# Kernel optimization log

Hardware: AMD Instinct MI355X
Metric: run time of the kernel (lower is better)

## Reference

```python
import jax, jax.numpy as jnp
import numpy as np

B, D, NH, HD = 32, 384, 8, 48
HP = WP = 14
N = HP * WP
L = 24
EPS_LN = 1e-5


def _ln(x, w, b):
    m = jnp.mean(x, -1, keepdims=True)
    v = jnp.mean((x - m) ** 2, -1, keepdims=True)
    return (x - m) * jax.lax.rsqrt(v + EPS_LN) * w + b


def _gelu(x):
    return jax.nn.gelu(x, approximate=False)


def _conv(x, w, s, p, groups=1):
    return jax.lax.conv_general_dilated(x, w, (s, s), [(p, p), (p, p)],
        dimension_numbers=('NCHW', 'OIHW', 'NCHW'), feature_group_count=groups)


def _bn(x, g, b):
    # eval-mode BatchNorm2d with running_mean=0, running_var=1
    scale = g * jax.lax.rsqrt(jnp.asarray(1.0 + 1e-5, x.dtype))
    return x * scale[None, :, None, None] + b[None, :, None, None]


def _pos_embed(pos_w, pos_b):
    two_pi = 2.0 * np.pi
    y = (jnp.arange(HP, dtype=jnp.float32) + 1.0) / ((HP + 1e-6) * two_pi)
    xg = (jnp.arange(WP, dtype=jnp.float32) + 1.0) / ((WP + 1e-6) * two_pi)
    y_embed = jnp.broadcast_to(y[:, None], (HP, WP))
    x_embed = jnp.broadcast_to(xg[None, :], (HP, WP))
    dim_t = 10000.0 ** (2.0 * (jnp.arange(32) // 2).astype(jnp.float32) / 32.0)
    px = x_embed[..., None] / dim_t  # [H,W,32]
    py = y_embed[..., None] / dim_t
    px = jnp.stack([jnp.sin(px[..., 0::2]), jnp.cos(px[..., 1::2])], -1).reshape(HP, WP, 32)
    py = jnp.stack([jnp.sin(py[..., 0::2]), jnp.cos(py[..., 1::2])], -1).reshape(HP, WP, 32)
    pos = jnp.concatenate([py, px], -1)  # [H,W,64]
    pos = jnp.einsum('hwc,dc->hwd', pos, pos_w[:, :, 0, 0]) + pos_b
    return pos.reshape(1, N, D)


def _xca_block(t, p):
    Bc = t.shape[0]
    h = _ln(t, p['n1_w'], p['n1_b'])
    qkv = (h @ p['qkv_w'].T + p['qkv_b']).reshape(Bc, N, 3, NH, HD)
    q = qkv[:, :, 0].transpose(0, 2, 3, 1)  # [B,H,d,N]
    k = qkv[:, :, 1].transpose(0, 2, 3, 1)
    v = qkv[:, :, 2].transpose(0, 2, 3, 1)
    q = q / jnp.maximum(jnp.linalg.norm(q, axis=-1, keepdims=True), 1e-12)
    k = k / jnp.maximum(jnp.linalg.norm(k, axis=-1, keepdims=True), 1e-12)
    attn = jnp.einsum('bhdn,bhen->bhde', q, k) * p['temp'][None, :, None, None]
    a = jax.nn.softmax(attn, -1)  # channel-wise softmax over d_h
    o = jnp.einsum('bhde,bhen->bnhd', a, v).reshape(Bc, N, D)
    o = o @ p['proj_w'].T + p['proj_b']
    t = t + p['g1'] * o
    h = _ln(t, p['n3_w'], p['n3_b']).transpose(0, 2, 1).reshape(Bc, D, HP, WP)
    h = _conv(h, p['lpi1_w'], 1, 1, groups=D) + p['lpi1_b'][None, :, None, None]
    h = _bn(_gelu(h), p['lpi_bn_g'], p['lpi_bn_b'])
    h = _conv(h, p['lpi2_w'], 1, 1, groups=D) + p['lpi2_b'][None, :, None, None]
    t = t + p['g3'] * h.reshape(Bc, D, N).transpose(0, 2, 1)
    h = _ln(t, p['n2_w'], p['n2_b'])
    h = _gelu(h @ p['fc1_w'].T + p['fc1_b']) @ p['fc2_w'].T + p['fc2_b']
    return t + p['g2'] * h


def _ca_block(t, p):
    Bc, Nc, _ = t.shape
    h = _ln(t, p['n1_w'], p['n1_b'])
    qkv = (h @ p['qkv_w'].T + p['qkv_b']).reshape(Bc, Nc, 3, NH, HD)
    q = qkv[:, :, 0].transpose(0, 2, 1, 3)  # [B,H,N,d]
    k = qkv[:, :, 1].transpose(0, 2, 1, 3)
    v = qkv[:, :, 2].transpose(0, 2, 1, 3)
    attn = jnp.sum(q[:, :, :1] * k, -1) * (HD ** -0.5)  # [B,H,N]
    a = jax.nn.softmax(attn, -1)
    cls = jnp.einsum('bhn,bhnd->bhd', a, v).reshape(Bc, 1, D)
    cls = cls @ p['proj_w'].T + p['proj_b']
    attn_out = jnp.concatenate([cls, h[:, 1:]], 1)
    t = t + p['g1'] * attn_out
    t = _ln(t, p['n2_w'], p['n2_b'])
    res = t
    cls2 = _gelu(t[:, :1] @ p['fc1_w'].T + p['fc1_b']) @ p['fc2_w'].T + p['fc2_b']
    return jnp.concatenate([p['g2'] * cls2, t[:, 1:]], 1) + res


def setup_inputs() -> dict:
    key = jax.random.key(0)
    k = iter(jax.random.split(key, 64))
    def rn(shape, std=0.02):
        return jax.random.normal(next(k), shape, jnp.float32) * std
    inp = {}
    inp['x'] = jax.random.normal(next(k), (B, 3, 224, 224), jnp.float32)
    inp['cls_token'] = rn((1, 1, D))
    inp['pos_w'] = rn((D, 64, 1, 1))
    inp['pos_b'] = jnp.zeros((D,))
    for i, (co, ci) in enumerate([(48, 3), (96, 48), (192, 96), (384, 192)], 1):
        inp['pe_w%d' % i] = rn((co, ci, 3, 3))
        inp['pe_g%d' % i] = jnp.ones((co,))
        inp['pe_b%d' % i] = jnp.zeros((co,))
    inp['xqkv_w'] = rn((L, 3 * D, D)); inp['xqkv_b'] = jnp.zeros((L, 3 * D))
    inp['xproj_w'] = rn((L, D, D)); inp['xproj_b'] = jnp.zeros((L, D))
    inp['xtemp'] = jnp.ones((L, NH))
    for n in ('n1', 'n2', 'n3'):
        inp['x%s_w' % n] = jnp.ones((L, D)); inp['x%s_b' % n] = jnp.zeros((L, D))
    inp['xfc1_w'] = rn((L, 4 * D, D)); inp['xfc1_b'] = jnp.zeros((L, 4 * D))
    inp['xfc2_w'] = rn((L, D, 4 * D)); inp['xfc2_b'] = jnp.zeros((L, D))
    inp['xlpi1_w'] = rn((L, D, 1, 3, 3), 0.1); inp['xlpi1_b'] = jnp.zeros((L, D))
    inp['xlpi2_w'] = rn((L, D, 1, 3, 3), 0.1); inp['xlpi2_b'] = jnp.zeros((L, D))
    inp['xbn_g'] = jnp.ones((L, D)); inp['xbn_b'] = jnp.zeros((L, D))
    for g in ('g1', 'g2', 'g3'):
        inp['x%s' % g] = jnp.full((L, D), 1e-5)
    L2 = 2
    inp['cqkv_w'] = rn((L2, 3 * D, D)); inp['cqkv_b'] = jnp.zeros((L2, 3 * D))
    inp['cproj_w'] = rn((L2, D, D)); inp['cproj_b'] = jnp.zeros((L2, D))
    for n in ('n1', 'n2'):
        inp['c%s_w' % n] = jnp.ones((L2, D)); inp['c%s_b' % n] = jnp.zeros((L2, D))
    inp['cfc1_w'] = rn((L2, 4 * D, D)); inp['cfc1_b'] = jnp.zeros((L2, 4 * D))
    inp['cfc2_w'] = rn((L2, D, 4 * D)); inp['cfc2_b'] = jnp.zeros((L2, D))
    inp['cg1'] = jnp.full((L2, D), 1e-5); inp['cg2'] = jnp.full((L2, D), 1e-5)
    inp['norm_w'] = jnp.ones((D,)); inp['norm_b'] = jnp.zeros((D,))
    inp['head_w'] = rn((1000, D)); inp['head_b'] = jnp.zeros((1000,))
    return inp


def reference(x, cls_token, pos_w, pos_b, pe_w1, pe_g1, pe_b1, pe_w2, pe_g2, pe_b2, pe_w3, pe_g3, pe_b3, pe_w4, pe_g4, pe_b4, xqkv_w, xqkv_b, xproj_w, xproj_b, xtemp, xn1_w, xn1_b, xn2_w, xn2_b, xn3_w, xn3_b, xfc1_w, xfc1_b, xfc2_w, xfc2_b, xlpi1_w, xlpi1_b, xlpi2_w, xlpi2_b, xbn_g, xbn_b, xg1, xg2, xg3, cqkv_w, cqkv_b, cproj_w, cproj_b, cn1_w, cn1_b, cn2_w, cn2_b, cfc1_w, cfc1_b, cfc2_w, cfc2_b, cg1, cg2, norm_w, norm_b, head_w, head_b):
    h = _gelu(_bn(_conv(x, pe_w1, 2, 1), pe_g1, pe_b1))
    h = _gelu(_bn(_conv(h, pe_w2, 2, 1), pe_g2, pe_b2))
    h = _gelu(_bn(_conv(h, pe_w3, 2, 1), pe_g3, pe_b3))
    h = _bn(_conv(h, pe_w4, 2, 1), pe_g4, pe_b4)  # [B,D,14,14]
    t = h.reshape(h.shape[0], D, N).transpose(0, 2, 1)  # [B,N,D]
    t = t + _pos_embed(pos_w, pos_b)
    xca = {'qkv_w': xqkv_w, 'qkv_b': xqkv_b, 'proj_w': xproj_w, 'proj_b': xproj_b,
           'temp': xtemp, 'n1_w': xn1_w, 'n1_b': xn1_b, 'n2_w': xn2_w, 'n2_b': xn2_b,
           'n3_w': xn3_w, 'n3_b': xn3_b, 'fc1_w': xfc1_w, 'fc1_b': xfc1_b,
           'fc2_w': xfc2_w, 'fc2_b': xfc2_b, 'lpi1_w': xlpi1_w, 'lpi1_b': xlpi1_b,
           'lpi2_w': xlpi2_w, 'lpi2_b': xlpi2_b, 'lpi_bn_g': xbn_g, 'lpi_bn_b': xbn_b,
           'g1': xg1, 'g2': xg2, 'g3': xg3}
    t, _ = jax.lax.scan(lambda c, p: (_xca_block(c, p), None), t, xca)
    t = jnp.concatenate([jnp.broadcast_to(cls_token, (t.shape[0], 1, D)), t], 1)
    for i in range(2):
        p = {'qkv_w': cqkv_w[i], 'qkv_b': cqkv_b[i], 'proj_w': cproj_w[i],
             'proj_b': cproj_b[i], 'n1_w': cn1_w[i], 'n1_b': cn1_b[i],
             'n2_w': cn2_w[i], 'n2_b': cn2_b[i], 'fc1_w': cfc1_w[i],
             'fc1_b': cfc1_b[i], 'fc2_w': cfc2_w[i], 'fc2_b': cfc2_b[i],
             'g1': cg1[i], 'g2': cg2[i]}
        t = _ca_block(t, p)
    t = _ln(t, norm_w, norm_b)[:, 0]
    return t @ head_w.T + head_b
```

## Files before the change

### kernel.cpp

```cpp
#include <hip/hip_runtime.h>
#include <hip/hip_bf16.h>

#define B_ 32
#define D_ 384
#define N_ 196
#define NH_ 8
#define HD_ 48
#define L_ 24

typedef __bf16 bf16x8 __attribute__((ext_vector_type(8)));
typedef __bf16 bf16x4 __attribute__((ext_vector_type(4)));
typedef float f32x4 __attribute__((ext_vector_type(4)));

__device__ __forceinline__ float gelu_f(float v){
    return 0.5f * v * (1.0f + erff(v * 0.70710678118654752f));
}

__global__ __launch_bounds__(256) void cvt_bf(const float* __restrict__ s, __bf16* __restrict__ d, long n){
    long i = ((long)blockIdx.x * 256 + threadIdx.x) * 8;
    if (i >= n) return;
    float4 a = *reinterpret_cast<const float4*>(s + i);
    float4 b = *reinterpret_cast<const float4*>(s + i + 4);
    bf16x8 r;
    r[0] = (__bf16)a.x; r[1] = (__bf16)a.y; r[2] = (__bf16)a.z; r[3] = (__bf16)a.w;
    r[4] = (__bf16)b.x; r[5] = (__bf16)b.y; r[6] = (__bf16)b.z; r[7] = (__bf16)b.w;
    *reinterpret_cast<bf16x8*>(d + i) = r;
}

__global__ __launch_bounds__(256) void cvt_pad(const float* __restrict__ s, __bf16* __restrict__ d,
                                               int rows, int K, int rows_pad){
    int id = blockIdx.x * 256 + threadIdx.x;
    if (id >= rows_pad * K) return;
    int r = id / K;
    d[id] = (r < rows) ? (__bf16)s[id] : (__bf16)0.f;
}

__global__ __launch_bounds__(256) void wprep(const float* __restrict__ w, __bf16* __restrict__ W2,
                                             int Co, int Ci, int Kpad){
    int id = blockIdx.x * 256 + threadIdx.x;
    if (id >= Co * Kpad) return;
    int co = id / Kpad, k = id - co * Kpad;
    float v = 0.f;
    if (k < 9 * Ci){
        int tap = k / Ci, ci = k - tap * Ci;
        v = w[((long)co * Ci + ci) * 9 + tap];
    }
    W2[id] = (__bf16)v;
}

__global__ __launch_bounds__(256) void im2col_x(const float* __restrict__ x, __bf16* __restrict__ A){
    int id = blockIdx.x * 256 + threadIdx.x;
    if (id >= 401408) return;
    int ox = id % 112; int t1 = id / 112; int oy = t1 % 112; int b = t1 / 112;
    __bf16 buf[32];
    #pragma unroll
    for (int i = 0; i < 32; i++) buf[i] = (__bf16)0.f;
    const float* xb = x + (long)b * 3 * 224 * 224;
    #pragma unroll
    for (int tap = 0; tap < 9; tap++){
        int ky = tap / 3, kx = tap % 3;
        int iy = oy * 2 - 1 + ky, ix = ox * 2 - 1 + kx;
        if ((unsigned)iy < 224u && (unsigned)ix < 224u){
            #pragma unroll
            for (int ci = 0; ci < 3; ci++)
                buf[tap * 3 + ci] = (__bf16)xb[((long)ci * 224 + iy) * 224 + ix];
        }
    }
    __bf16* dst = A + (long)id * 32;
    #pragma unroll
    for (int i = 0; i < 4; i++)
        *reinterpret_cast<bf16x8*>(dst + i * 8) = *reinterpret_cast<bf16x8*>(buf + i * 8);
}

__global__ __launch_bounds__(256) void im2col_bf(const __bf16* __restrict__ in, __bf16* __restrict__ A,
                                                 int C, int Hi, int Wi, int Ho, int Wo, int Kpad, int total){
    int id = blockIdx.x * 256 + threadIdx.x;
    if (id >= total) return;
    int tap = id % 9; int pix = id / 9;
    int ox = pix % Wo; int t1 = pix / Wo; int oy = t1 % Ho; int b = t1 / Ho;
    int ky = tap / 3, kx = tap % 3;
    int iy = oy * 2 - 1 + ky, ix = ox * 2 - 1 + kx;
    __bf16* dst = A + (long)pix * Kpad + tap * C;
    if ((unsigned)iy < (unsigned)Hi && (unsigned)ix < (unsigned)Wi){
        const __bf16* src = in + ((long)(b * Hi + iy) * Wi + ix) * C;
        for (int c = 0; c < C; c += 8)
            *reinterpret_cast<bf16x8*>(dst + c) = *reinterpret_cast<const bf16x8*>(src + c);
    } else {
        bf16x8 z{};
        for (int c = 0; c < C; c += 8) *reinterpret_cast<bf16x8*>(dst + c) = z;
    }
    if (tap == 0){
        bf16x8 z{};
        for (int c = 9 * C; c < Kpad; c += 8)
            *reinterpret_cast<bf16x8*>(A + (long)pix * Kpad + c) = z;
    }
}

template<int GELU, int POSOUT>
__global__ __launch_bounds__(256) void gemm_conv(const __bf16* __restrict__ A, int Kpad,
                                                 const __bf16* __restrict__ W,
                                                 const float* __restrict__ g, const float* __restrict__ bb,
                                                 void* __restrict__ Cv, int N,
                                                 const float* __restrict__ pos){
    __shared__ __align__(16) char smem[20480];
    char* Ab = smem;
    char* Bb = smem + 10240;
    const int tid  = threadIdx.x;
    const int lane = tid & 63;
    const int wn   = (tid >> 6) & 1;
    const int wm   = tid >> 7;
    const int row0 = blockIdx.x * 128;
    const int col0 = blockIdx.y * 128;
    const int hi = lane >> 4, lo = lane & 15;
    f32x4 acc[4][4] = {};
    auto loadA = [&](int kk, int i)->bf16x8 {
        int p = i * 256 + tid;
        int r = p >> 2, cq = p & 3;
// ... 142 lines not shown
            int c = c0 + j;
            yb[(long)c * 196] = (__bf16)((v[j] - m) * r * n3w[c] + n3b[c]);
        }
    }
}

__global__ __launch_bounds__(128) void ln2res(float* __restrict__ t,
                                              const __bf16* __restrict__ hadd,
                                              const float* __restrict__ n2w, const float* __restrict__ n2b,
                                              __bf16* __restrict__ h){
    long row = blockIdx.x;
    int tid = threadIdx.x;
    int c0 = tid * 4;
    float v[4] = {0.f, 0.f, 0.f, 0.f};
    if (tid < 96){
        float4 tv = *reinterpret_cast<const float4*>(t + row * 384 + c0);
        bf16x4 hv = *reinterpret_cast<const bf16x4*>(hadd + row * 384 + c0);
        v[0] = tv.x + (float)hv[0];
        v[1] = tv.y + (float)hv[1];
        v[2] = tv.z + (float)hv[2];
        v[3] = tv.w + (float)hv[3];
        *reinterpret_cast<float4*>(t + row * 384 + c0) = make_float4(v[0], v[1], v[2], v[3]);
    }
    float s = v[0] + v[1] + v[2] + v[3];
    float ss = v[0] * v[0] + v[1] * v[1] + v[2] * v[2] + v[3] * v[3];
    for (int off = 32; off; off >>= 1){ s += __shfl_down(s, off); ss += __shfl_down(ss, off); }
    __shared__ float rs[2], rss[2];
    if ((tid & 63) == 0){ rs[tid >> 6] = s; rss[tid >> 6] = ss; }
    __syncthreads();
    float S = rs[0] + rs[1], SS = rss[0] + rss[1];
    float m = S * (1.0f / 384.0f);
    float var = SS * (1.0f / 384.0f) - m * m;
    float r = rsqrtf(var + 1e-5f);
    if (tid < 96){
        bf16x4 o;
        #pragma unroll
        for (int j = 0; j < 4; j++){
            int c = c0 + j;
            o[j] = (__bf16)((v[j] - m) * r * n2w[c] + n2b[c]);
        }
        *reinterpret_cast<bf16x4*>(h + row * 384 + c0) = o;
    }
}

__global__ __launch_bounds__(128) void fc2_res_ln(const __bf16* __restrict__ f2,
                                                  const float* __restrict__ g2,
                                                  float* __restrict__ t,
                                                  const float* __restrict__ n1w, const float* __restrict__ n1b,
                                                  __bf16* __restrict__ h){
    long row = blockIdx.x;
    int tid = threadIdx.x;
    int c0 = tid * 4;
    float v[4] = {0.f, 0.f, 0.f, 0.f};
    if (tid < 96){
        float4 tv = *reinterpret_cast<const float4*>(t + row * 384 + c0);
        bf16x4 fv = *reinterpret_cast<const bf16x4*>(f2 + row * 384 + c0);
        v[0] = tv.x + g2[c0 + 0] * (float)fv[0];
        v[1] = tv.y + g2[c0 + 1] * (float)fv[1];
        v[2] = tv.z + g2[c0 + 2] * (float)fv[2];
        v[3] = tv.w + g2[c0 + 3] * (float)fv[3];
        *reinterpret_cast<float4*>(t + row * 384 + c0) = make_float4(v[0], v[1], v[2], v[3]);
    }
    float s = v[0] + v[1] + v[2] + v[3];
    float ss = v[0] * v[0] + v[1] * v[1] + v[2] * v[2] + v[3] * v[3];
    for (int off = 32; off; off >>= 1){ s += __shfl_down(s, off); ss += __shfl_down(ss, off); }
    __shared__ float rs[2], rss[2];
    if ((tid & 63) == 0){ rs[tid >> 6] = s; rss[tid >> 6] = ss; }
    __syncthreads();
    float S = rs[0] + rs[1], SS = rss[0] + rss[1];
    float m = S * (1.0f / 384.0f);
    float var = SS * (1.0f / 384.0f) - m * m;
    float r = rsqrtf(var + 1e-5f);
    if (tid < 96){
        bf16x4 o;
        #pragma unroll
        for (int j = 0; j < 4; j++){
            int c = c0 + j;
            o[j] = (__bf16)((v[j] - m) * r * n1w[c] + n1b[c]);
        }
        *reinterpret_cast<bf16x4*>(h + row * 384 + c0) = o;
    }
}

template<int MODE, int OUTBF, int ACVT, int GUARD, int NGUARD>
__global__ __launch_bounds__(256) void gemm_bb2(const void* __restrict__ Av, long lda,
                                                const __bf16* __restrict__ W, int Kw,
                                                const float* __restrict__ bias,
                                                void* __restrict__ Cv, long ldc,
                                                int K, int M, int Ncols){
    __shared__ __align__(16) char smem[27648];
    char* Ab = smem;
    char* Bb = smem + 9216;
    const int tid = threadIdx.x;
    const int lane = tid & 63;
    const int wn = tid >> 6;
    const int row0 = blockIdx.x * 64;
    const int col0 = blockIdx.y * 128;
    const int hi = lane >> 4, lo = lane & 15;
    const __bf16* Abf = (const __bf16*)Av;
    const float* Af = (const float*)Av;
    f32x4 acc[4][2] = {};
    auto loadA = [&](int kk, int i)->bf16x8 {
        int p = i * 256 + tid;
        int r = p >> 3, cq = p & 7;
        bf16x8 va{};
        int grow = row0 + r;
        if (!GUARD || grow < M){
            long ai = (long)grow * lda + kk + cq * 8;
            if (ACVT){
                float4 a0 = *reinterpret_cast<const float4*>(Af + ai);
                float4 a1 = *reinterpret_cast<const float4*>(Af + ai + 4);
                va[0] = (__bf16)a0.x; va[1] = (__bf16)a0.y; va[2] = (__bf16)a0.z; va[3] = (__bf16)a0.w;
                va[4] = (__bf16)a1.x; va[5] = (__bf16)a1.y; va[6] = (__bf16)a1.z; va[7] = (__bf16)a1.w;
            } else {
                va = *reinterpret_cast<const bf16x8*>(Abf + ai);
            }
        }
        return va;
    };
    auto loadB = [&](int kk, int i)->bf16x8 {
        int p = i * 256 + tid;
        int r = p >> 3, cq = p & 7;
        return *reinterpret_cast<const bf16x8*>(W + (long)(col0 + r) * Kw + kk + cq * 8);
    };
    bf16x8 vaC[2], vwC[4];
    vaC[0] = loadA(0, 0); vaC[1] = loadA(0, 1);
    #pragma unroll
    for (int i = 0; i < 4; i++) vwC[i] = loadB(0, i);
    for (int k0 = 0; k0 < K; k0 += 64){
        #pragma unroll
        for (int i = 0; i < 2; i++){
            int p = i * 256 + tid;
            int r = p >> 3, cq = p & 7;
            *reinterpret_cast<bf16x8*>(Ab + r * 144 + cq * 16) = vaC[i];
        }
        #pragma unroll
        for (int i = 0; i < 4; i++){
            int p = i * 256 + tid;
            int r = p >> 3, cq = p & 7;
            *reinterpret_cast<bf16x8*>(Bb + r * 144 + cq * 16) = vwC[i];
        }
        __syncthreads();
        int kn = (k0 + 64 < K) ? k0 + 64 : k0;
        bf16x8 vaN[2], vwN[4];
        vaN[0] = loadA(kn, 0); vaN[1] = loadA(kn, 1);
        #pragma unroll
        for (int i = 0; i < 4; i++) vwN[i] = loadB(kn, i);
        bf16x8 af[2][4], bfr[2][2];
        #pragma unroll
        for (int m = 0; m < 4; m++){
            af[0][m] = *reinterpret_cast<const bf16x8*>(Ab + (m * 16 + lo) * 144 + hi * 16);
            af[1][m] = *reinterpret_cast<const bf16x8*>(Ab + (m * 16 + lo) * 144 + 64 + hi * 16);
        }
        #pragma unroll
        for (int n = 0; n < 2; n++){
            bfr[0][n] = *reinterpret_cast<const bf16x8*>(Bb + (wn * 32 + n * 16 + lo) * 144 + hi * 16);
            bfr[1][n] = *reinterpret_cast<const bf16x8*>(Bb + (wn * 32 + n * 16 + lo) * 144 + 64 + hi * 16);
        }
        #pragma unroll
        for (int kc = 0; kc < 2; kc++)
            #pragma unroll
            for (int m = 0; m < 4; m++)
                #pragma unroll
                for (int n = 0; n < 2; n++)
                    acc[m][n] = __builtin_amdgcn_mfma_f32_16x16x32_bf16(af[kc][m], bfr[kc][n], acc[m][n], 0, 0, 0);
        __syncthreads();
        vaC[0] = vaN[0]; vaC[1] = vaN[1];
        #pragma unroll
        for (int i = 0; i < 4; i++) vwC[i] = vwN[i];
    }
    float* Cf = (float*)Cv;
    __bf16* Cb = (__bf16*)Cv;
    #pragma unroll
    for (int m = 0; m < 4; m++){
        #pragma unroll
        for (int n = 0; n < 2; n++){
            int row = row0 + m * 16 + hi * 4;
            int col = col0 + wn * 32 + n * 16 + lo;
            if (NGUARD && col >= Ncols) continue;
            float bv = bias[col];
            #pragma unroll
            for (int j = 0; j < 4; j++){
                if (GUARD && (row + j) >= M) continue;
                float v = acc[m][n][j] + bv;
                if (MODE == 1) v = gelu_f(v);
                long ci = (long)(row + j) * ldc + col;
                if (OUTBF) Cb[ci] = (__bf16)v;
                else Cf[ci] = v;
            }
        }
    }
}

__global__ __launch_bounds__(256) void gemm_bb3(const __bf16* __restrict__ A, long lda,
                                                const __bf16* __restrict__ W, int Kw,
                                                const float* __restrict__ bias,
                                                __bf16* __restrict__ C, long ldc,
                                                int K){
    __shared__ __align__(16) char smem[18432];
    char* Ab = smem;
    char* Bb = smem + 9216;
    const int tid = threadIdx.x;
    const int lane = tid & 63;
    const int wid = tid >> 6;
    const int wm = wid >> 1, wnn = wid & 1;
    const int row0 = blockIdx.x * 64;
    const int col0 = blockIdx.y * 64;
    const int hi = lane >> 4, lo = lane & 15;
    f32x4 acc[2][2] = {};
    auto loadA = [&](int kk, int i)->bf16x8 {
        int p = i * 256 + tid;
        int r = p >> 3, cq = p & 7;
        return *reinterpret_cast<const bf16x8*>(A + (long)(row0 + r) * lda + kk + cq * 8);
    };
    auto loadB = [&](int kk, int i)->bf16x8 {
        int p = i * 256 + tid;
        int r = p >> 3, cq = p & 7;
        return *reinterpret_cast<const bf16x8*>(W + (long)(col0 + r) * Kw + kk + cq * 8);
    };
    bf16x8 vaC[2], vwC[2];
    vaC[0] = loadA(0, 0); vaC[1] = loadA(0, 1);
    vwC[0] = loadB(0, 0); vwC[1] = loadB(0, 1);
    for (int k0 = 0; k0 < K; k0 += 64){
        #pragma unroll
        for (int i = 0; i < 2; i++){
            int p = i * 256 + tid;
            int r = p >> 3, cq = p & 7;
            *reinterpret_cast<bf16x8*>(Ab + r * 144 + cq * 16) = vaC[i];
            *reinterpret_cast<bf16x8*>(Bb + r * 144 + cq * 16) = vwC[i];
        }
        __syncthreads();
        int kn = (k0 + 64 < K) ? k0 + 64 : k0;
        bf16x8 vaN[2], vwN[2];
        vaN[0] = loadA(kn, 0); vaN[1] = loadA(kn, 1);
        vwN[0] = loadB(kn, 0); vwN[1] = loadB(kn, 1);
        bf16x8 af[2][2], bfr[2][2];
        #pragma unroll
        for (int m = 0; m < 2; m++){
            af[0][m] = *reinterpret_cast<const bf16x8*>(Ab + (wm * 32 + m * 16 + lo) * 144 + hi * 16);
            af[1][m] = *reinterpret_cast<const bf16x8*>(Ab + (wm * 32 + m * 16 + lo) * 144 + 64 + hi * 16);
        }
        #pragma unroll
        for (int n = 0; n < 2; n++){
            bfr[0][n] = *reinterpret_cast<const bf16x8*>(Bb + (wnn * 32 + n * 16 + lo) * 144 + hi * 16);
            bfr[1][n] = *reinterpret_cast<const bf16x8*>(Bb + (wnn * 32 + n * 16 + lo) * 144 + 64 + hi * 16);
        }
        #pragma unroll
        for (int kc = 0; kc < 2; kc++)
            #pragma unroll
            for (int m = 0; m < 2; m++)
                #pragma unroll
                for (int n = 0; n < 2; n++)
                    acc[m][n] = __builtin_amdgcn_mfma_f32_16x16x32_bf16(af[kc][m], bfr[kc][n], acc[m][n], 0, 0, 0);
        __syncthreads();
        vaC[0] = vaN[0]; vaC[1] = vaN[1]; vwC[0] = vwN[0]; vwC[1] = vwN[1];
    }
    #pragma unroll
    for (int m = 0; m < 2; m++){
        #pragma unroll
        for (int n = 0; n < 2; n++){
            int row = row0 + wm * 32 + m * 16 + hi * 4;
            int col = col0 + wnn * 32 + n * 16 + lo;
            float bv = bias[col];
            #pragma unroll
            for (int j = 0; j < 4; j++)
                C[(long)(row + j) * ldc + col] = (__bf16)(acc[m][n][j] + bv);
        }
    }
}

__global__ __launch_bounds__(384) void pos_embed(const float* __restrict__ pw, const float* __restrict__ pb,
                                                 float* __restrict__ pos){
    __shared__ float p64[64];
    int n = blockIdx.x;
    int iy = n / 14, ix = n % 14;
    int t = threadIdx.x;
    if (t < 64){
        int axis = t >> 5;
        int c = t & 31;
        int u = c >> 1;
        float coord = (axis == 0) ? (float)(iy + 1) : (float)(ix + 1);
        float val = coord / ((14.0f + 1e-6f) * 6.283185307179586f);
        float T = powf(10000.0f, (float)u / 16.0f);
        float a = val / T;
        p64[t] = (c & 1) ? cosf(a) : sinf(a);
    }
    __syncthreads();
    float acc = 0.f;
    const float* wr = pw + (long)t * 64;
    #pragma unroll 8
    for (int c = 0; c < 64; c++) acc += p64[c] * wr[c];
    pos[n * 384 + t] = acc + pb[t];
}

__global__ __launch_bounds__(256) void xca2(const __bf16* __restrict__ qkv, const float* __restrict__ temp,
                                            __bf16* __restrict__ o){
    __shared__ __align__(16) char smem[45056];
    __bf16* qs = (__bf16*)smem;
    __bf16* ks = (__bf16*)(smem + 22272);
    float* inq = (float*)(smem + 44544);
    float* ink = (float*)(smem + 44736);
    float* att = (float*)smem;
    __bf16* abf = (__bf16*)(smem + 22272);
    int bh = blockIdx.x;
    int b = bh >> 3, h = bh & 7;
    const int tid = threadIdx.x;
    const int wid = tid >> 6, lane = tid & 63;
    const int hi = lane >> 4, lo = lane & 15;
    const __bf16* base = qkv + ((long)b * 196) * 1152 + h * 48;
    bf16x8 z8 = {};
    for (int idx = tid; idx < 48 * 28; idx += 256){
        int d = idx / 28, n = 196 + idx % 28;
        qs[d * 232 + n] = (__bf16)0.f;
        ks[d * 232 + n] = (__bf16)0.f;
    }
    for (int ch = tid; ch < 196 * 6; ch += 256){
        int n = ch / 6, c = ch % 6, d0 = c * 8;
        bf16x8 q8 = *reinterpret_cast<const bf16x8*>(base + (long)n * 1152 + d0);
        bf16x8 k8 = *reinterpret_cast<const bf16x8*>(base + (long)n * 1152 + 384 + d0);
        #pragma unroll
        for (int j = 0; j < 8; j++){
            qs[(d0 + j) * 232 + n] = q8[j];
            ks[(d0 + j) * 232 + n] = k8[j];
        }
    }
    __syncthreads();
    for (int r = wid; r < 48; r += 4){
        float sq = 0.f, sk = 0.f;
        for (int n = lane; n < 196; n += 64){
            float qv = (float)qs[r * 232 + n];
            float kv = (float)ks[r * 232 + n];
            sq += qv * qv; sk += kv * kv;
        }
        for (int off = 32; off; off >>= 1){ sq += __shfl_down(sq, off); sk += __shfl_down(sk, off); }
        if (lane == 0){
            inq[r] = 1.0f / fmaxf(sqrtf(sq), 1e-12f);
            ink[r] = 1.0f / fmaxf(sqrtf(sk), 1e-12f);
        }
    }
    __syncthreads();
    float tempv = temp[h];
    f32x4 qk0 = {}, qk1 = {}, qk2 = {};
    __builtin_amdgcn_s_setprio(1);
    {
        int mi = wid / 3, ni = wid % 3;
        #pragma unroll
        for (int k0 = 0; k0 < 224; k0 += 32){
            bf16x8 af = *reinterpret_cast<const bf16x8*>(qs + (mi * 16 + lo) * 232 + k0 + hi * 8);
            bf16x8 bf = *reinterpret_cast<const bf16x8*>(ks + (ni * 16 + lo) * 232 + k0 + hi * 8);
            qk0 = __builtin_amdgcn_mfma_f32_16x16x32_bf16(af, bf, qk0, 0, 0, 0);
        }
    }
    {
        int tt = wid + 4;
        int mi = tt / 3, ni = tt % 3;
        #pragma unroll
        for (int k0 = 0; k0 < 224; k0 += 32){
            bf16x8 af = *reinterpret_cast<const bf16x8*>(qs + (mi * 16 + lo) * 232 + k0 + hi * 8);
            bf16x8 bf = *reinterpret_cast<const bf16x8*>(ks + (ni * 16 + lo) * 232 + k0 + hi * 8);
            qk1 = __builtin_amdgcn_mfma_f32_16x16x32_bf16(af, bf, qk1, 0, 0, 0);
        }
    }
    if (wid == 0){
        #pragma unroll
        for (int k0 = 0; k0 < 224; k0 += 32){
            bf16x8 af = *reinterpret_cast<const bf16x8*>(qs + (2 * 16 + lo) * 232 + k0 + hi * 8);
            bf16x8 bf = *reinterpret_cast<const bf16x8*>(ks + (2 * 16 + lo) * 232 + k0 + hi * 8);
            qk2 = __builtin_amdgcn_mfma_f32_16x16x32_bf16(af, bf, qk2, 0, 0, 0);
        }
    }
    __builtin_amdgcn_s_setprio(0);
    __syncthreads();
    {
        int mi = wid / 3, ni = wid % 3;
        int e = ni * 16 + lo;
        float se = ink[e] * tempv;
        #pragma unroll
        for (int j = 0; j < 4; j++){
            int d = mi * 16 + hi * 4 + j;
            att[d * 68 + e] = qk0[j] * inq[d] * se;
        }
    }
    {
        int tt = wid + 4;
        int mi = tt / 3, ni = tt % 3;
        int e = ni * 16 + lo;
        float se = ink[e] * tempv;
        #pragma unroll
        for (int j = 0; j < 4; j++){
            int d = mi * 16 + hi * 4 + j;
            att[d * 68 + e] = qk1[j] * inq[d] * se;
        }
    }
    if (wid == 0){
        int e = 2 * 16 + lo;
        float se = ink[e] * tempv;
        #pragma unroll
        for (int j = 0; j < 4; j++){
            int d = 2 * 16 + hi * 4 + j;
            att[d * 68 + e] = qk2[j] * inq[d] * se;
        }
    }
    __syncthreads();
    if (tid < 192){
        int r = tid >> 2, q4 = tid & 3;
        const float* row = att + r * 68 + q4 * 12;
        float mx = -1e30f;
        #pragma unroll
        for (int i = 0; i < 12; i++) mx = fmaxf(mx, row[i]);
        mx = fmaxf(mx, __shfl_xor(mx, 1));
        mx = fmaxf(mx, __shfl_xor(mx, 2));
        float pv[12]; float sm = 0.f;
        #pragma unroll
        for (int i = 0; i < 12; i++){ pv[i] = expf(row[i] - mx); sm += pv[i]; }
        sm += __shfl_xor(sm, 1);
        sm += __shfl_xor(sm, 2);
        float inv = 1.0f / sm;
        #pragma unroll
        for (int i = 0; i < 12; i++) abf[r * 72 + q4 * 12 + i] = (__bf16)(pv[i] * inv);
    }
    for (int idx = tid; idx < 48 * 3; idx += 256){
        int r = idx / 3, c = 48 + (idx % 3) * 8;
        *reinterpret_cast<bf16x8*>(abf + r * 72 + c) = z8;
    }
    __syncthreads();
    __bf16* ob = o + ((long)b * 196) * 384 + h * 48;
    __builtin_amdgcn_s_setprio(1);
    for (int tt = wid; tt < 39; tt += 4){
        int mi = tt / 13, ni = tt % 13;
        int nB = ni * 16 + lo;
        const __bf16* vrow = base + (long)nB * 1152 + 768;
        f32x4 acc = {};
        #pragma unroll
        for (int e0 = 0; e0 < 64; e0 += 32){
            bf16x8 af = *reinterpret_cast<const bf16x8*>(abf + (mi * 16 + lo) * 72 + e0 + hi * 8);
            bf16x8 bf = *reinterpret_cast<const bf16x8*>(vrow + e0 + hi * 8);
            acc = __builtin_amdgcn_mfma_f32_16x16x32_bf16(af, bf, acc, 0, 0, 0);
        }
        int n = nB;
        if (n < 196){
            #pragma unroll
            for (int j = 0; j < 4; j++){
                int d = mi * 16 + hi * 4 + j;
                ob[(long)n * 384 + d] = (__bf16)acc[j];
            }
        }
    }
    __builtin_amdgcn_s_setprio(0);
}

__global__ __launch_bounds__(256) void lpi_g(const __bf16* __restrict__ ht,
                                             const float* __restrict__ w1, const float* __restrict__ b1,
                                             const float* __restrict__ bng, const float* __restrict__ bnb,
                                             const float* __restrict__ w2, const float* __restrict__ b2,
                                             const float* __restrict__ g3, __bf16* __restrict__ hadd){
    int bd = blockIdx.x;
    int d = bd % 384, b = bd / 384;
    __shared__ float p[16][16];
    __shared__ float p2[16][16];
    __shared__ float wA[9], wB[9];
    int tt = threadIdx.x;
    int yy = tt / 16, xx = tt % 16;
    p[yy][xx] = 0.f; p2[yy][xx] = 0.f;
    if (tt < 9){ wA[tt] = w1[d * 9 + tt]; wB[tt] = w2[d * 9 + tt]; }
    __syncthreads();
    if (tt < 196){
        int y = tt / 14, x = tt % 14;
        p[y + 1][x + 1] = (float)ht[((long)b * 384 + d) * 196 + tt];
    }
    __syncthreads();
    if (tt < 196){
        int y = tt / 14, x = tt % 14;
        float a = 0.f;
        #pragma unroll
        for (int ky = 0; ky < 3; ky++)
            #pragma unroll
            for (int kx = 0; kx < 3; kx++)
                a += wA[ky * 3 + kx] * p[y + ky][x + kx];
        a += b1[d];
        a = gelu_f(a);
        a = a * (bng[d] * rsqrtf(1.0f + 1e-5f)) + bnb[d];
        p2[y + 1][x + 1] = a;
    }
    __syncthreads();
    if (tt < 196){
        int y = tt / 14, x = tt % 14;
        float a = 0.f;
        #pragma unroll
        for (int ky = 0; ky < 3; ky++)
            #pragma unroll
            for (int kx = 0; kx < 3; kx++)
                a += wB[ky * 3 + kx] * p2[y + ky][x + kx];
        a += b2[d];
        hadd[((long)b * 196 + tt) * 384 + d] = (__bf16)(g3[d] * a);
    }
}

__global__ __launch_bounds__(256) void concat_cls(const float* __restrict__ t, const float* __restrict__ clstok,
                                                  float* __restrict__ tc){
    long i = (long)blockIdx.x * 256 + threadIdx.x;
    if (i >= (long)B_ * 197 * 384) return;
    int d = (int)(i % 384);
    long bn = i / 384;
    int n = (int)(bn % 197);
    int b = (int)(bn / 197);
    tc[i] = (n == 0) ? clstok[d] : t[((long)b * 196 + (n - 1)) * 384 + d];
}

__global__ __launch_bounds__(256) void ca_attn(const __bf16* __restrict__ qkv, float* __restrict__ clsp){
    int bh = blockIdx.x;
    int b = bh >> 3, h = bh & 7;
    const __bf16* base = qkv + (long)b * 197 * 1152 + h * 48;
    __shared__ float q0[48];
    __shared__ float at2[197];
    __shared__ float smax, ssum;
    int tid = threadIdx.x;
    if (tid < 48) q0[tid] = (float)base[tid];
    __syncthreads();
    if (tid < 197){
        const __bf16* kr = base + (long)tid * 1152 + 384;
        float s = 0.f;
        for (int d = 0; d < 48; d++) s += q0[d] * (float)kr[d];
        at2[tid] = s * rsqrtf(48.0f);
    }
    __syncthreads();
    if (tid == 0){
        float m = -1e30f;
// ... 36 lines not shown
    int d = (int)(i % 384);
    long bn = i / 384;
    int n = (int)(bn % 197);
    int b = (int)(bn / 197);
    float hv = hc[i];
    tc[i] = (n == 0) ? (g2[d] * cls2[b * 384 + d] + hv) : (hv + hv);
}

extern "C" void kernel_launch(void* const* d_in, const int* in_sizes, int n_in,
                              void* d_out, int out_size, void* d_ws, size_t ws_size,
                              hipStream_t stream){
    (void)in_sizes; (void)n_in; (void)out_size; (void)ws_size;
    const float* x      = (const float*)d_in[0];
    const float* clstok = (const float*)d_in[1];
    const float* pos_w  = (const float*)d_in[2];
    const float* pos_b  = (const float*)d_in[3];
    const float* pe_w[4] = {(const float*)d_in[4], (const float*)d_in[7], (const float*)d_in[10], (const float*)d_in[13]};
    const float* pe_g[4] = {(const float*)d_in[5], (const float*)d_in[8], (const float*)d_in[11], (const float*)d_in[14]};
    const float* pe_b[4] = {(const float*)d_in[6], (const float*)d_in[9], (const float*)d_in[12], (const float*)d_in[15]};
    const float* xqkv_w = (const float*)d_in[16];
    const float* xqkv_b = (const float*)d_in[17];
    const float* xproj_w = (const float*)d_in[18];
    const float* xproj_b = (const float*)d_in[19];
    const float* xtemp  = (const float*)d_in[20];
    const float* xn1_w = (const float*)d_in[21];
    const float* xn1_b = (const float*)d_in[22];
    const float* xn2_w = (const float*)d_in[23];
    const float* xn2_b = (const float*)d_in[24];
    const float* xn3_w = (const float*)d_in[25];
    const float* xn3_b = (const float*)d_in[26];
    const float* xfc1_w = (const float*)d_in[27];
    const float* xfc1_b = (const float*)d_in[28];
    const float* xfc2_w = (const float*)d_in[29];
    const float* xfc2_b = (const float*)d_in[30];
    const float* xlpi1_w = (const float*)d_in[31];
    const float* xlpi1_b = (const float*)d_in[32];
    const float* xlpi2_w = (const float*)d_in[33];
    const float* xlpi2_b = (const float*)d_in[34];
    const float* xbn_g = (const float*)d_in[35];
    const float* xbn_b = (const float*)d_in[36];
    const float* xg1 = (const float*)d_in[37];
    const float* xg2 = (const float*)d_in[38];
    const float* xg3 = (const float*)d_in[39];
    const float* cqkv_w = (const float*)d_in[40];
    const float* cqkv_b = (const float*)d_in[41];
    const float* cproj_w = (const float*)d_in[42];
    const float* cproj_b = (const float*)d_in[43];
    const float* cn1_w = (const float*)d_in[44];
    const float* cn1_b = (const float*)d_in[45];
    const float* cn2_w = (const float*)d_in[46];
    const float* cn2_b = (const float*)d_in[47];
    const float* cfc1_w = (const float*)d_in[48];
    const float* cfc1_b = (const float*)d_in[49];
    const float* cfc2_w = (const float*)d_in[50];
    const float* cfc2_b = (const float*)d_in[51];
    const float* cg1 = (const float*)d_in[52];
    const float* cg2 = (const float*)d_in[53];
    const float* norm_w = (const float*)d_in[54];
    const float* norm_b = (const float*)d_in[55];
    const float* head_w = (const float*)d_in[56];
    const float* head_b = (const float*)d_in[57];
    float* outp = (float*)d_out;

    float* ws = (float*)d_ws;
    __bf16* A1   = (__bf16*)(ws);
    __bf16* A2   = (__bf16*)(ws);
    __bf16* A3   = (__bf16*)(ws);
    __bf16* A4   = (__bf16*)(ws);
    __bf16* out1 = (__bf16*)(ws + 22500000L);
    __bf16* out2 = (__bf16*)(ws + 22500000L);
    __bf16* out3 = (__bf16*)(ws + 27400000L);
    __bf16* wcv  = (__bf16*)(ws + 36000000L);
    __bf16* W1c = wcv;
    __bf16* W2c = wcv + 1536;
    __bf16* W3c = wcv + 44544;
    __bf16* W4c = wcv + 216576;
    __bf16* wqkv_bf = (__bf16*)(ws);
    __bf16* wproj_bf = (__bf16*)(ws + 5308416L);
    __bf16* wfc1_bf = (__bf16*)(ws + 7077888L);
    __bf16* wfc2_bf = (__bf16*)(ws + 14155776L);
    float*  t       = ws + 21233664L;
    float*  pos     = ws + 23642112L;
    __bf16* h_bf    = (__bf16*)(ws + 23717376L);
    __bf16* qkv_bf  = (__bf16*)(ws + 24921600L);
    __bf16* o_bf    = (__bf16*)(ws + 28534272L);
    __bf16* ht_bf   = (__bf16*)(ws + 29738496L);
    __bf16* f1_bf   = (__bf16*)(ws + 32146944L);
    __bf16* o2_bf   = (__bf16*)(ws + 34555392L);
    __bf16* f2_bf   = (__bf16*)(ws + 24921600L);
    __bf16* hadd_bf = (__bf16*)(ws + 28534272L);
    float* tc   = ws;
    float* hc   = ws + 2420736L;
    __bf16* qkvc_bf = (__bf16*)(ws + 4841472L);
    float* clsp = ws + 8472576L;
    float* clso = clsp + 12288;
    float* f1c  = clso + 12288;
    float* cls2 = f1c + 49152;
    float* clsf = cls2 + 12288;
    __bf16* cqkv_bf  = (__bf16*)(ws + 9000000L);
    __bf16* cproj_bf = (__bf16*)(ws + 9500000L);
    __bf16* cfc1_bf  = (__bf16*)(ws + 9800000L);
    __bf16* cfc2_bf  = (__bf16*)(ws + 10400000L);
    __bf16* headw_bf = (__bf16*)(ws + 11000000L);

    wprep<<<(48 * 32 + 255) / 256, 256, 0, stream>>>(pe_w[0], W1c, 48, 3, 32);
    wprep<<<(96 * 448 + 255) / 256, 256, 0, stream>>>(pe_w[1], W2c, 96, 48, 448);
    wprep<<<(192 * 896 + 255) / 256, 256, 0, stream>>>(pe_w[2], W3c, 192, 96, 896);
    wprep<<<(384 * 1728 + 255) / 256, 256, 0, stream>>>(pe_w[3], W4c, 384, 192, 1728);

    im2col_x<<<1568, 256, 0, stream>>>(x, A1);
    { dim3 g(3136, 1); gemm_conv<1, 0><<<g, 256, 0, stream>>>(A1, 32, W1c, pe_g[0], pe_b[0], out1, 48, nullptr); }
    im2col_bf<<<(100352 * 9 + 255) / 256, 256, 0, stream>>>(out1, A2, 48, 112, 112, 56, 56, 448, 100352 * 9);
    { dim3 g(784, 1); gemm_conv<1, 0><<<g, 256, 0, stream>>>(A2, 448, W2c, pe_g[1], pe_b[1], out2, 96, nullptr); }
    im2col_bf<<<(25088 * 9 + 255) / 256, 256, 0, stream>>>(out2, A3, 96, 56, 56, 28, 28, 896, 25088 * 9);
    pos_embed<<<196, 384, 0, stream>>>(pos_w, pos_b, pos);
    { dim3 g(196, 2); gemm_conv<1, 0><<<g, 256, 0, stream>>>(A3, 896, W3c, pe_g[2], pe_b[2], out3, 192, nullptr); }
    im2col_bf<<<(6272 * 9 + 255) / 256, 256, 0, stream>>>(out3, A4, 192, 28, 28, 14, 14, 1728, 6272 * 9);
    { dim3 g(49, 3); gemm_conv<0, 1><<<g, 256, 0, stream>>>(A4, 1728, W4c, pe_g[3], pe_b[3], t, 384, pos); }

    {
        long n1 = (long)L_ * 1152 * 384;
        long n2 = (long)L_ * 384 * 384;
        long n3 = (long)L_ * 1536 * 384;
        cvt_bf<<<(int)((n1 + 2047) / 2048), 256, 0, stream>>>(xqkv_w, wqkv_bf, n1);
        cvt_bf<<<(int)((n2 + 2047) / 2048), 256, 0, stream>>>(xproj_w, wproj_bf, n2);
        cvt_bf<<<(int)((n3 + 2047) / 2048), 256, 0, stream>>>(xfc1_w, wfc1_bf, n3);
        cvt_bf<<<(int)((n3 + 2047) / 2048), 256, 0, stream>>>(xfc2_w, wfc2_bf, n3);
    }

    const int M = B_ * N_;
    ln384_bf<<<M, 128, 0, stream>>>(t, xn1_w, xn1_b, h_bf);
    for (int l = 0; l < L_; l++){
        {
            dim3 g(98, 9);
            gemm_bb2<0, 1, 0, 0, 0><<<g, 256, 0, stream>>>(h_bf, 384, wqkv_bf + (long)l * 1152 * 384, 384,
                                                           xqkv_b + l * 1152, qkv_bf, 1152, 384, M, 0);
        }
        xca2<<<B_ * NH_, 256, 0, stream>>>(qkv_bf, xtemp + l * 8, o_bf);
        {
            dim3 g(98, 6);
            gemm_bb3<<<g, 256, 0, stream>>>(o_bf, 384, wproj_bf + (long)l * 384 * 384, 384,
                                            xproj_b + l * 384, o2_bf, 384, 384);
        }
        proj_res_lnt<<<M, 128, 0, stream>>>(o2_bf, xg1 + l * 384, t,
                                            xn3_w + l * 384, xn3_b + l * 384, ht_bf);
        lpi_g<<<B_ * D_, 256, 0, stream>>>(ht_bf, xlpi1_w + (long)l * 384 * 9, xlpi1_b + l * 384,
                                           xbn_g + l * 384, xbn_b + l * 384,
                                           xlpi2_w + (long)l * 384 * 9, xlpi2_b + l * 384,
                                           xg3 + l * 384, hadd_bf);
        ln2res<<<M, 128, 0, stream>>>(t, hadd_bf, xn2_w + l * 384, xn2_b + l * 384, h_bf);
        {
            dim3 g(98, 12);
            gemm_bb2<1, 1, 0, 0, 0><<<g, 256, 0, stream>>>(h_bf, 384, wfc1_bf + (long)l * 1536 * 384, 384,
                                                           xfc1_b + l * 1536, f1_bf, 1536, 384, M, 0);
        }
        {
            dim3 g(98, 6);
            gemm_bb3<<<g, 256, 0, stream>>>(f1_bf, 1536, wfc2_bf + (long)l * 1536 * 384, 1536,
                                            xfc2_b + l * 384, f2_bf, 384, 1536);
        }
        int ln = (l + 1) % L_;
        fc2_res_ln<<<M, 128, 0, stream>>>(f2_bf, xg2 + l * 384, t,
                                          xn1_w + ln * 384, xn1_b + ln * 384, h_bf);
    }

    const long NC = (long)B_ * 197 * 384;
    concat_cls<<<(int)(NC / 256), 256, 0, stream>>>(t, clstok, tc);
    {
        long nc = (long)2 * 1152 * 384;
        cvt_bf<<<(int)((nc + 2047) / 2048), 256, 0, stream>>>(cqkv_w, cqkv_bf, nc);
        long np = (long)2 * 384 * 384;
        cvt_bf<<<(int)((np + 2047) / 2048), 256, 0, stream>>>(cproj_w, cproj_bf, np);
        long nf = (long)2 * 1536 * 384;
        cvt_bf<<<(int)((nf + 2047) / 2048), 256, 0, stream>>>(cfc1_w, cfc1_bf, nf);
        cvt_bf<<<(int)((nf + 2047) / 2048), 256, 0, stream>>>(cfc2_w, cfc2_bf, nf);
        cvt_pad<<<(1024 * 384 + 255) / 256, 256, 0, stream>>>(head_w, headw_bf, 1000, 384, 1024);
    }
    const int MC = B_ * 197;
    for (int i = 0; i < 2; i++){
        ln384<<<MC, 128, 0, stream>>>(tc, 384, cn1_w + i * 384, cn1_b + i * 384, hc, 384);
        {
            dim3 g(99, 9);
            gemm_bb2<0, 1, 1, 1, 0><<<g, 256, 0, stream>>>(hc, 384, cqkv_bf + (long)i * 1152 * 384, 384,
                                                           cqkv_b + i * 1152, qkvc_bf, 1152, 384, MC, 0);
        }
        ca_attn<<<B_ * NH_, 256, 0, stream>>>(qkvc_bf, clsp);
        {
            dim3 g(1, 3);
            gemm_bb2<0, 0, 1, 1, 0><<<g, 256, 0, stream>>>(clsp, 384, cproj_bf + (long)i * 384 * 384, 384,
                                                           cproj_b + i * 384, clso, 384, 384, 32, 0);
        }
        ca_update1<<<(int)(NC / 256), 256, 0, stream>>>(clso, hc, cg1 + i * 384, tc);
        ln384<<<MC, 128, 0, stream>>>(tc, 384, cn2_w + i * 384, cn2_b + i * 384, hc, 384);
        {
            dim3 g(1, 12);
            gemm_bb2<1, 0, 1, 1, 0><<<g, 256, 0, stream>>>(hc, (long)197 * 384, cfc1_bf + (long)i * 1536 * 384, 384,
                                                           cfc1_b + i * 1536, f1c, 1536, 384, 32, 0);
        }
        {
            dim3 g(1, 3);
            gemm_bb2<0, 0, 1, 1, 0><<<g, 256, 0, stream>>>(f1c, 1536, cfc2_bf + (long)i * 1536 * 384, 1536,
                                                           cfc2_b + i * 384, cls2, 384, 1536, 32, 0);
        }
        ca_update2<<<(int)(NC / 256), 256, 0, stream>>>(cls2, hc, cg2 + i * 384, tc);
    }

    ln384<<<32, 128, 0, stream>>>(tc, (long)197 * 384, norm_w, norm_b, clsf, 384);
    {
        dim3 g(1, 8);
        gemm_bb2<0, 0, 1, 1, 1><<<g, 256, 0, stream>>>(clsf, 384, headw_bf, 384,
                                                       head_b, outp, 1000, 384, 32, 1000);
    }
}
```

Measured before the change: 3.932 ms.

## Write QKV GEMM output as transposed Q/K planes and read attention operands from global

The QKV GEMM epilogue now scatters Q and K into per-(batch,head) transposed [d][224] buffers, zero-padded once, and V into a separate contiguous buffer. The XCA kernel drops its shared-memory transpose staging and reads MFMA operands and norms straight from global memory. This removes the in-kernel transpose and one barrier, and shrinks shared memory so more blocks can be resident. The cost is strided, uncoalesced scalar stores in the GEMM epilogue and unstaged global loads feeding the MFMAs.

```diff
diff --git a/kernel.cpp b/kernel.cpp
--- a/kernel.cpp
+++ b/kernel.cpp
@@ -33,6 +33,15 @@
     if (id >= rows_pad * K) return;
     int r = id / K;
     d[id] = (r < rows) ? (__bf16)s[id] : (__bf16)0.f;
+}
+
+__global__ __launch_bounds__(256) void zero_qkt_pad(__bf16* __restrict__ qt, __bf16* __restrict__ kt){
+    int id = blockIdx.x * 256 + threadIdx.x;
+    if (id >= 32 * 8 * 48 * 28) return;
+    int n = 196 + id % 28;
+    int r = id / 28;
+    qt[(long)r * 224 + n] = (__bf16)0.f;
+    kt[(long)r * 224 + n] = (__bf16)0.f;
 }
 
 __global__ __launch_bounds__(256) void wprep(const float* __restrict__ w, __bf16* __restrict__ W2,
@@ -341,12 +350,14 @@
     }
 }
 
-template<int MODE, int OUTBF, int ACVT, int GUARD, int NGUARD>
+template<int MODE, int OUTBF, int ACVT, int GUARD, int NGUARD, int QKVOUT>
 __global__ __launch_bounds__(256) void gemm_bb2(const void* __restrict__ Av, long lda,
                                                 const __bf16* __restrict__ W, int Kw,
                                                 const float* __restrict__ bias,
                                                 void* __restrict__ Cv, long ldc,
-                                                int K, int M, int Ncols){
+                                                int K, int M, int Ncols,
+                                                __bf16* __restrict__ qtp, __bf16* __restrict__ ktp,
+                                                __bf16* __restrict__ vp){
     __shared__ __align__(16) char smem[27648];
     char* Ab = smem;
     char* Bb = smem + 9216;
@@ -443,9 +454,23 @@
                 if (GUARD && (row + j) >= M) continue;
                 float v = acc[m][n][j] + bv;
                 if (MODE == 1) v = gelu_f(v);
-                long ci = (long)(row + j) * ldc + col;
-                if (OUTBF) Cb[ci] = (__bf16)v;
-                else Cf[ci] = v;
+                if (QKVOUT){
+                    int rowj = row + j;
+                    if (col < 768){
+                        int qk = (col >= 384);
+                        int c = col - qk * 384;
+                        int hh = c / 48, dd = c - hh * 48;
+                        int bb = rowj / 196, nn = rowj - bb * 196;
+                        __bf16* dst = qk ? ktp : qtp;
+                        dst[(((long)bb * 8 + hh) * 48 + dd) * 224 + nn] = (__bf16)v;
+                    } else {
+                        vp[(long)rowj * 384 + (col - 768)] = (__bf16)v;
+                    }
+                } else {
+                    long ci = (long)(row + j) * ldc + col;
+                    if (OUTBF) Cb[ci] = (__bf16)v;
+                    else Cf[ci] = v;
+                }
             }
         }
     }
@@ -552,44 +577,29 @@
     pos[n * 384 + t] = acc + pb[t];
 }
 
-__global__ __launch_bounds__(256) void xca2(const __bf16* __restrict__ qkv, const float* __restrict__ temp,
+__global__ __launch_bounds__(256) void xca3(const __bf16* __restrict__ qt, const __bf16* __restrict__ kt,
+                                            const __bf16* __restrict__ v, const float* __restrict__ temp,
                                             __bf16* __restrict__ o){
-    __shared__ __align__(16) char smem[45056];
-    __bf16* qs = (__bf16*)smem;
-    __bf16* ks = (__bf16*)(smem + 22272);
-    float* inq = (float*)(smem + 44544);
-    float* ink = (float*)(smem + 44736);
-    float* att = (float*)smem;
-    __bf16* abf = (__bf16*)(smem + 22272);
+    __shared__ __align__(16) float att[48 * 68];
+    __shared__ __align__(16) __bf16 abf[48 * 72];
+    __shared__ float inq[48], ink[48];
     int bh = blockIdx.x;
     int b = bh >> 3, h = bh & 7;
     const int tid = threadIdx.x;
     const int wid = tid >> 6, lane = tid & 63;
     const int hi = lane >> 4, lo = lane & 15;
-    const __bf16* base = qkv + ((long)b * 196) * 1152 + h * 48;
-    bf16x8 z8 = {};
-    for (int idx = tid; idx < 48 * 28; idx += 256){
-        int d = idx / 28, n = 196 + idx % 28;
-        qs[d * 232 + n] = (__bf16)0.f;
-        ks[d * 232 + n] = (__bf16)0.f;
-    }
-    for (int ch = tid; ch < 196 * 6; ch += 256){
-        int n = ch / 6, c = ch % 6, d0 = c * 8;
-        bf16x8 q8 = *reinterpret_cast<const bf16x8*>(base + (long)n * 1152 + d0);
-        bf16x8 k8 = *reinterpret_cast<const bf16x8*>(base + (long)n * 1152 + 384 + d0);
-        #pragma unroll
-        for (int j = 0; j < 8; j++){
-            qs[(d0 + j) * 232 + n] = q8[j];
-            ks[(d0 + j) * 232 + n] = k8[j];
-        }
-    }
-    __syncthreads();
+    const __bf16* qb = qt + (long)bh * 48 * 224;
+    const __bf16* kb = kt + (long)bh * 48 * 224;
     for (int r = wid; r < 48; r += 4){
         float sq = 0.f, sk = 0.f;
-        for (int n = lane; n < 196; n += 64){
-            float qv = (float)qs[r * 232 + n];
-            float kv = (float)ks[r * 232 + n];
-            sq += qv * qv; sk += kv * kv;
+        if (lane < 56){
+            bf16x4 q4 = *reinterpret_cast<const bf16x4*>(qb + r * 224 + lane * 4);
+            bf16x4 k4 = *reinterpret_cast<const bf16x4*>(kb + r * 224 + lane * 4);
+            #pragma unroll
+            for (int j = 0; j < 4; j++){
+                float qv = (float)q4[j], kv = (float)k4[j];
+                sq += qv * qv; sk += kv * kv;
+            }
         }
         for (int off = 32; off; off >>= 1){ sq += __shfl_down(sq, off); sk += __shfl_down(sk, off); }
         if (lane == 0){
@@ -597,7 +607,6 @@
             ink[r] = 1.0f / fmaxf(sqrtf(sk), 1e-12f);
         }
     }
-    __syncthreads();
     float tempv = temp[h];
     f32x4 qk0 = {}, qk1 = {}, qk2 = {};
     __builtin_amdgcn_s_setprio(1);
@@ -605,8 +614,8 @@
         int mi = wid / 3, ni = wid % 3;
         #pragma unroll
         for (int k0 = 0; k0 < 224; k0 += 32){
-            bf16x8 af = *reinterpret_cast<const bf16x8*>(qs + (mi * 16 + lo) * 232 + k0 + hi * 8);
-            bf16x8 bf = *reinterpret_cast<const bf16x8*>(ks + (ni * 16 + lo) * 232 + k0 + hi * 8);
+            bf16x8 af = *reinterpret_cast<const bf16x8*>(qb + (mi * 16 + lo) * 224 + k0 + hi * 8);
+            bf16x8 bf = *reinterpret_cast<const bf16x8*>(kb + (ni * 16 + lo) * 224 + k0 + hi * 8);
             qk0 = __builtin_amdgcn_mfma_f32_16x16x32_bf16(af, bf, qk0, 0, 0, 0);
         }
     }
@@ -615,16 +624,16 @@
         int mi = tt / 3, ni = tt % 3;
         #pragma unroll
         for (int k0 = 0; k0 < 224; k0 += 32){
-            bf16x8 af = *reinterpret_cast<const bf16x8*>(qs + (mi * 16 + lo) * 232 + k0 + hi * 8);
-            bf16x8 bf = *reinterpret_cast<const bf16x8*>(ks + (ni * 16 + lo) * 232 + k0 + hi * 8);
+            bf16x8 af = *reinterpret_cast<const bf16x8*>(qb + (mi * 16 + lo) * 224 + k0 + hi * 8);
+            bf16x8 bf = *reinterpret_cast<const bf16x8*>(kb + (ni * 16 + lo) * 224 + k0 + hi * 8);
             qk1 = __builtin_amdgcn_mfma_f32_16x16x32_bf16(af, bf, qk1, 0, 0, 0);
         }
     }
     if (wid == 0){
         #pragma unroll
         for (int k0 = 0; k0 < 224; k0 += 32){
-            bf16x8 af = *reinterpret_cast<const bf16x8*>(qs + (2 * 16 + lo) * 232 + k0 + hi * 8);
-            bf16x8 bf = *reinterpret_cast<const bf16x8*>(ks + (2 * 16 + lo) * 232 + k0 + hi * 8);
+            bf16x8 af = *reinterpret_cast<const bf16x8*>(qb + (2 * 16 + lo) * 224 + k0 + hi * 8);
+            bf16x8 bf = *reinterpret_cast<const bf16x8*>(kb + (2 * 16 + lo) * 224 + k0 + hi * 8);
             qk2 = __builtin_amdgcn_mfma_f32_16x16x32_bf16(af, bf, qk2, 0, 0, 0);
         }
     }
@@ -678,9 +687,12 @@
         #pragma unroll
         for (int i = 0; i < 12; i++) abf[r * 72 + q4 * 12 + i] = (__bf16)(pv[i] * inv);
     }
-    for (int idx = tid; idx < 48 * 3; idx += 256){
-        int r = idx / 3, c = 48 + (idx % 3) * 8;
-        *reinterpret_cast<bf16x8*>(abf + r * 72 + c) = z8;
+    {
+        bf16x8 z8{};
+        for (int idx = tid; idx < 48 * 3; idx += 256){
+            int r = idx / 3, c = 48 + (idx % 3) * 8;
+            *reinterpret_cast<bf16x8*>(abf + r * 72 + c) = z8;
+        }
     }
     __syncthreads();
     __bf16* ob = o + ((long)b * 196) * 384 + h * 48;
@@ -688,7 +700,7 @@
     for (int tt = wid; tt < 39; tt += 4){
         int mi = tt / 13, ni = tt % 13;
         int nB = ni * 16 + lo;
-        const __bf16* vrow = base + (long)nB * 1152 + 768;
+        const __bf16* vrow = v + ((long)b * 196 + nB) * 384 + h * 48;
         f32x4 acc = {};
         #pragma unroll
         for (int e0 = 0; e0 < 64; e0 += 32){
@@ -696,12 +708,11 @@
             bf16x8 bf = *reinterpret_cast<const bf16x8*>(vrow + e0 + hi * 8);
             acc = __builtin_amdgcn_mfma_f32_16x16x32_bf16(af, bf, acc, 0, 0, 0);
         }
-        int n = nB;
-        if (n < 196){
+        if (nB < 196){
             #pragma unroll
             for (int j = 0; j < 4; j++){
                 int d = mi * 16 + hi * 4 + j;
-                ob[(long)n * 384 + d] = (__bf16)acc[j];
+                ob[(long)nB * 384 + d] = (__bf16)acc[j];
             }
         }
     }
@@ -904,13 +915,15 @@
     float*  t       = ws + 21233664L;
     float*  pos     = ws + 23642112L;
     __bf16* h_bf    = (__bf16*)(ws + 23717376L);
-    __bf16* qkv_bf  = (__bf16*)(ws + 24921600L);
-    __bf16* o_bf    = (__bf16*)(ws + 28534272L);
+    __bf16* qt_bf   = (__bf16*)(ws + 24921600L);
+    __bf16* kt_bf   = (__bf16*)(ws + 26297856L);
+    __bf16* v_bf    = (__bf16*)(ws + 27674112L);
     __bf16* ht_bf   = (__bf16*)(ws + 29738496L);
+    __bf16* o_bf    = (__bf16*)(ws + 30942720L);
     __bf16* f1_bf   = (__bf16*)(ws + 32146944L);
     __bf16* o2_bf   = (__bf16*)(ws + 34555392L);
     __bf16* f2_bf   = (__bf16*)(ws + 24921600L);
-    __bf16* hadd_bf = (__bf16*)(ws + 28534272L);
+    __bf16* hadd_bf = (__bf16*)(ws + 30942720L);
     float* tc   = ws;
     float* hc   = ws + 2420736L;
     __bf16* qkvc_bf = (__bf16*)(ws + 4841472L);
@@ -948,6 +961,7 @@
         cvt_bf<<<(int)((n2 + 2047) / 2048), 256, 0, stream>>>(xproj_w, wproj_bf, n2);
         cvt_bf<<<(int)((n3 + 2047) / 2048), 256, 0, stream>>>(xfc1_w, wfc1_bf, n3);
         cvt_bf<<<(int)((n3 + 2047) / 2048), 256, 0, stream>>>(xfc2_w, wfc2_bf, n3);
+        zero_qkt_pad<<<(32 * 8 * 48 * 28 + 255) / 256, 256, 0, stream>>>(qt_bf, kt_bf);
     }
 
     const int M = B_ * N_;
@@ -955,10 +969,11 @@
     for (int l = 0; l < L_; l++){
         {
             dim3 g(98, 9);
-            gemm_bb2<0, 1, 0, 0, 0><<<g, 256, 0, stream>>>(h_bf, 384, wqkv_bf + (long)l * 1152 * 384, 384,
-                                                           xqkv_b + l * 1152, qkv_bf, 1152, 384, M, 0);
-        }
-        xca2<<<B_ * NH_, 256, 0, stream>>>(qkv_bf, xtemp + l * 8, o_bf);
+            gemm_bb2<0, 1, 0, 0, 0, 1><<<g, 256, 0, stream>>>(h_bf, 384, wqkv_bf + (long)l * 1152 * 384, 384,
+                                                              xqkv_b + l * 1152, nullptr, 0, 384, M, 0,
+                                                              qt_bf, kt_bf, v_bf);
+        }
+        xca3<<<B_ * NH_, 256, 0, stream>>>(qt_bf, kt_bf, v_bf, xtemp + l * 8, o_bf);
         {
             dim3 g(98, 6);
             gemm_bb3<<<g, 256, 0, stream>>>(o_bf, 384, wproj_bf + (long)l * 384 * 384, 384,
@@ -973,8 +988,9 @@
         ln2res<<<M, 128, 0, stream>>>(t, hadd_bf, xn2_w + l * 384, xn2_b + l * 384, h_bf);
         {
             dim3 g(98, 12);
-            gemm_bb2<1, 1, 0, 0, 0><<<g, 256, 0, stream>>>(h_bf, 384, wfc1_bf + (long)l * 1536 * 384, 384,
-                                                           xfc1_b + l * 1536, f1_bf, 1536, 384, M, 0);
+            gemm_bb2<1, 1, 0, 0, 0, 0><<<g, 256, 0, stream>>>(h_bf, 384, wfc1_bf + (long)l * 1536 * 384, 384,
+                                                              xfc1_b + l * 1536, f1_bf, 1536, 384, M, 0,
+                                                              nullptr, nullptr, nullptr);
         }
         {
             dim3 g(98, 6);
@@ -1003,26 +1019,30 @@
         ln384<<<MC, 128, 0, stream>>>(tc, 384, cn1_w + i * 384, cn1_b + i * 384, hc, 384);
         {
             dim3 g(99, 9);
-            gemm_bb2<0, 1, 1, 1, 0><<<g, 256, 0, stream>>>(hc, 384, cqkv_bf + (long)i * 1152 * 384, 384,
-                                                           cqkv_b + i * 1152, qkvc_bf, 1152, 384, MC, 0);
+            gemm_bb2<0, 1, 1, 1, 0, 0><<<g, 256, 0, stream>>>(hc, 384, cqkv_bf + (long)i * 1152 * 384, 384,
+                                                              cqkv_b + i * 1152, qkvc_bf, 1152, 384, MC, 0,
+                                                              nullptr, nullptr, nullptr);
         }
         ca_attn<<<B_ * NH_, 256, 0, stream>>>(qkvc_bf, clsp);
         {
             dim3 g(1, 3);
-            gemm_bb2<0, 0, 1, 1, 0><<<g, 256, 0, stream>>>(clsp, 384, cproj_bf + (long)i * 384 * 384, 384,
-                                                           cproj_b + i * 384, clso, 384, 384, 32, 0);
+            gemm_bb2<0, 0, 1, 1, 0, 0><<<g, 256, 0, stream>>>(clsp, 384, cproj_bf + (long)i * 384 * 384, 384,
+                                                              cproj_b + i * 384, clso, 384, 384, 32, 0,
+                                                              nullptr, nullptr, nullptr);
         }
         ca_update1<<<(int)(NC / 256), 256, 0, stream>>>(clso, hc, cg1 + i * 384, tc);
         ln384<<<MC, 128, 0, stream>>>(tc, 384, cn2_w + i * 384, cn2_b + i * 384, hc, 384);
         {
             dim3 g(1, 12);
-            gemm_bb2<1, 0, 1, 1, 0><<<g, 256, 0, stream>>>(hc, (long)197 * 384, cfc1_bf + (long)i * 1536 * 384, 384,
-                                                           cfc1_b + i * 1536, f1c, 1536, 384, 32, 0);
+            gemm_bb2<1, 0, 1, 1, 0, 0><<<g, 256, 0, stream>>>(hc, (long)197 * 384, cfc1_bf + (long)i * 1536 * 384, 384,
+                                                              cfc1_b + i * 1536, f1c, 1536, 384, 32, 0,
+                                                              nullptr, nullptr, nullptr);
         }
         {
             dim3 g(1, 3);
-            gemm_bb2<0, 0, 1, 1, 0><<<g, 256, 0, stream>>>(f1c, 1536, cfc2_bf + (long)i * 1536 * 384, 1536,
-                                                           cfc2_b + i * 384, cls2, 384, 1536, 32, 0);
+            gemm_bb2<0, 0, 1, 1, 0, 0><<<g, 256, 0, stream>>>(f1c, 1536, cfc2_bf + (long)i * 1536 * 384, 1536,
+                                                              cfc2_b + i * 384, cls2, 384, 1536, 32, 0,
+                                                              nullptr, nullptr, nullptr);
         }
         ca_update2<<<(int)(NC / 256), 256, 0, stream>>>(cls2, hc, cg2 + i * 384, tc);
     }
@@ -1030,7 +1050,8 @@
     ln384<<<32, 128, 0, stream>>>(tc, (long)197 * 384, norm_w, norm_b, clsf, 384);
     {
         dim3 g(1, 8);
-        gemm_bb2<0, 0, 1, 1, 1><<<g, 256, 0, stream>>>(clsf, 384, headw_bf, 384,
-                                                       head_b, outp, 1000, 384, 32, 1000);
-    }
-}
+        gemm_bb2<0, 0, 1, 1, 1, 0><<<g, 256, 0, stream>>>(clsf, 384, headw_bf, 384,
+                                                          head_b, outp, 1000, 384, 32, 1000,
+                                                          nullptr, nullptr, nullptr);
+    }
+}
```

Measured after the change: 4.145 ms. 5.4% more time.
